# Kernel optimization log

Measured on AMD Instinct MI355X. Metric: run time of the kernel, lower is better.

Reference implementation:

```python
import jax, jax.numpy as jnp
import numpy as np

B, I, J, C = 1, 256, 256, 128
H, D = 4, 32          # no_heads, head_dim; c_hidden = H*D = 128
INF = 1.0e9
LN_EPS = 1e-5


def setup_inputs() -> dict:
    key = jax.random.key(0)
    ks = jax.random.split(key, 8)
    x = jax.random.normal(ks[0], (B, I, J, C), dtype=jnp.float32)
    mask = (jax.random.uniform(ks[1], (B, I, J)) > 0.1).astype(jnp.float32)
    std = 0.02
    wq = std * jax.random.normal(ks[2], (H * D, C), dtype=jnp.float32)
    wk = std * jax.random.normal(ks[3], (H * D, C), dtype=jnp.float32)
    wv = std * jax.random.normal(ks[4], (H * D, C), dtype=jnp.float32)
    wb = std * jax.random.normal(ks[5], (H, C), dtype=jnp.float32)
    wo = (std / np.sqrt(2 * H)) * jax.random.normal(ks[6], (C, H * D), dtype=jnp.float32)
    wo_b = jnp.zeros((C,), dtype=jnp.float32)
    ln_g = jnp.ones((C,), dtype=jnp.float32)
    ln_b = jnp.zeros((C,), dtype=jnp.float32)
    return {"x": x, "mask": mask, "ln_g": ln_g, "ln_b": ln_b,
            "wq": wq, "wk": wk, "wv": wv, "wb": wb, "wo": wo, "wo_b": wo_b}


def reference(x, mask, ln_g, ln_b, wq, wk, wv, wb, wo, wo_b):
    # LayerNorm over channel dim
    mu = jnp.mean(x, axis=-1, keepdims=True)
    var = jnp.mean(jnp.square(x - mu), axis=-1, keepdims=True)
    xn = (x - mu) * jax.lax.rsqrt(var + LN_EPS) * ln_g + ln_b

    # QKV projections (torch Linear: y = x @ W^T), reshape to heads
    q = (xn @ wq.T).reshape(B, I, J, H, D)
    k = (xn @ wk.T).reshape(B, I, J, H, D)
    v = (xn @ wv.T).reshape(B, I, J, H, D)

    scale = 1.0 / np.sqrt(D)
    # attention within each row i over the J dimension: [B, I, H, Jq, Jk]
    scores = jnp.einsum('biqhd,bikhd->bihqk', q, k) * scale

    # triangle bias: [B, I, J, H] -> [B, I, H, Jq, 1], broadcast over keys
    tb = jnp.einsum('bijc,hc->bijh', xn, wb)
    scores = scores + jnp.swapaxes(tb, -1, -2)[..., None]

    # mask bias: inf*(mask-1) -> [B, I, 1, Jq, 1] (as in the torch code)
    scores = scores + (INF * (mask - 1.0))[:, :, None, :, None]

    attn = jax.nn.softmax(scores, axis=-1)
    out = jnp.einsum('bihqk,bikhd->biqhd', attn, v).reshape(B, I, J, H * D)
    return out @ wo.T + wo_b
```

## Files before the change

kernel.cpp:

```cpp
#include <hip/hip_runtime.h>
#include <hip/hip_bf16.h>

typedef short bf16x8 __attribute__((ext_vector_type(8)));
typedef short bf16x4 __attribute__((ext_vector_type(4)));
typedef float f32x4  __attribute__((ext_vector_type(4)));

#define NI 256
#define NJ 256
#define NC 128
#define NH 4
#define ND 32

#define XN_OFF 0
#define XN_STR 272
#define Q_OFF  69632
#define K_OFF  90112
#define QK_STR 80
#define VT_OFF 110592
#define VT_STR 528
#define PB_OFF 127488
#define PB_STR 80
#define TB_OFF 137728
#define MB_OFF 141824
#define SMEM_BYTES 142848

__device__ __forceinline__ short f2bf(float f) {
    return __builtin_bit_cast(short, __float2bfloat16(f));
}
__device__ __forceinline__ float bf2f(short s) {
    unsigned u = ((unsigned)(unsigned short)s) << 16;
    return __builtin_bit_cast(float, u);
}

__global__ __launch_bounds__(512, 2)
void fta_fused(const float* __restrict__ x, const float* __restrict__ mask,
               const float* __restrict__ ln_g, const float* __restrict__ ln_b,
               const float* __restrict__ wq, const float* __restrict__ wk,
               const float* __restrict__ wv, const float* __restrict__ wb,
               const float* __restrict__ wo, const float* __restrict__ wo_b,
               float* __restrict__ out)
{
    extern __shared__ __align__(16) char smem[];
    const int tid  = threadIdx.x;
    const int lane = tid & 63;
    const int wid  = tid >> 6;
    const int g    = lane >> 4;
    const int l16  = lane & 15;
    const int i    = blockIdx.x;

    {
        const int t  = tid >> 1;
        const int ch = (tid & 1) * 64;
        const float* xr = x + ((size_t)i * NJ + t) * NC + ch;
        f32x4 vx[16];
        float s0 = 0.f;
        #pragma unroll
        for (int u = 0; u < 16; ++u) {
            vx[u] = *(const f32x4*)(xr + 4 * u);
            s0 += vx[u][0] + vx[u][1] + vx[u][2] + vx[u][3];
        }
        s0 += __shfl_xor(s0, 1);
        const float mu = s0 * (1.0f / 128.0f);
        float v0 = 0.f;
        #pragma unroll
        for (int u = 0; u < 16; ++u) {
            #pragma unroll
            for (int e = 0; e < 4; ++e) { float d = vx[u][e] - mu; v0 += d * d; }
        }
        v0 += __shfl_xor(v0, 1);
        const float rs = rsqrtf(v0 * (1.0f / 128.0f) + 1e-5f);
        short* xnrow = (short*)(smem + XN_OFF + (size_t)t * XN_STR) + ch;
        #pragma unroll
        for (int u = 0; u < 16; u += 2) {
            f32x4 ga = *(const f32x4*)(ln_g + ch + 4 * u);
            f32x4 gb = *(const f32x4*)(ln_g + ch + 4 * u + 4);
            f32x4 ba = *(const f32x4*)(ln_b + ch + 4 * u);
            f32x4 bb = *(const f32x4*)(ln_b + ch + 4 * u + 4);
            bf16x8 o8;
            #pragma unroll
            for (int e = 0; e < 4; ++e) {
                o8[e]     = f2bf((vx[u][e]     - mu) * rs * ga[e] + ba[e]);
                o8[4 + e] = f2bf((vx[u + 1][e] - mu) * rs * gb[e] + bb[e]);
            }
            *(bf16x8*)(xnrow + 4 * u) = o8;
        }
        if (tid < 256) {
            ((float*)(smem + MB_OFF))[tid] = 1.0e9f * (mask[(size_t)i * NJ + tid] - 1.0f);
        }
    }
    __syncthreads();

    for (int job = tid; job < NH * NJ; job += 512) {
        const int t = job & 255;
        const int h = job >> 8;
        const short* xnrow = (const short*)(smem + XN_OFF + (size_t)t * XN_STR);
        const float* wr = wb + h * NC;
        float acc = 0.f;
        #pragma unroll
        for (int c = 0; c < NC; c += 8) {
            bf16x8 xv = *(const bf16x8*)(xnrow + c);
            f32x4 wa = *(const f32x4*)(wr + c);
            f32x4 wz = *(const f32x4*)(wr + c + 4);
            acc += bf2f(xv[0]) * wa[0] + bf2f(xv[1]) * wa[1] + bf2f(xv[2]) * wa[2] + bf2f(xv[3]) * wa[3]
                 + bf2f(xv[4]) * wz[0] + bf2f(xv[5]) * wz[1] + bf2f(xv[6]) * wz[2] + bf2f(xv[7]) * wz[3];
        }
        ((float*)(smem + TB_OFF))[h * NJ + t] = acc;
    }

    f32x4 facc[2][8];
    #pragma unroll
    for (int qt = 0; qt < 2; ++qt)
        #pragma unroll
        for (int ct = 0; ct < 8; ++ct)
            facc[qt][ct] = (f32x4){0.f, 0.f, 0.f, 0.f};

    const float SCALE = 0.17677669529663687f;
    const f32x4 z4 = {0.f, 0.f, 0.f, 0.f};

    for (int h = 0; h < NH; ++h) {
        __syncthreads();
        for (int chunk = wid; chunk < 12; chunk += 8) {
            const int pn = chunk >> 1;
            const int mhalf = chunk & 1;
            const int p = pn >> 1;
            const int nt2 = pn & 1;
            const float* w = (p == 0) ? wq : ((p == 1) ? wk : wv);
            const int drow = h * ND + nt2 * 16 + l16;
            const float* wrow = w + (size_t)drow * NC + g * 8;
            bf16x8 bfr[4];
            #pragma unroll
            for (int ks = 0; ks < 4; ++ks) {
                f32x4 a = *(const f32x4*)(wrow + ks * 32);
                f32x4 b = *(const f32x4*)(wrow + ks * 32 + 4);
                bf16x8 t8;
                #pragma unroll
                for (int e = 0; e < 4; ++e) { t8[e] = f2bf(a[e]); t8[4 + e] = f2bf(b[e]); }
                bfr[ks] = t8;
            }
            for (int mt = 0; mt < 8; ++mt) {
                const int trow = mhalf * 128 + mt * 16;
                const short* xnr = (const short*)(smem + XN_OFF + (size_t)(trow + l16) * XN_STR) + g * 8;
                f32x4 acc = z4;
                #pragma unroll
                for (int ks = 0; ks < 4; ++ks) {
                    bf16x8 av = *(const bf16x8*)(xnr + ks * 32);
                    acc = __builtin_amdgcn_mfma_f32_16x16x32_bf16(av, bfr[ks], acc, 0, 0, 0);
                }
                const int tt = trow + g * 4;
                const int dd = nt2 * 16 + l16;
                if (p < 2) {
                    char* buf = smem + (p == 0 ? Q_OFF : K_OFF);
                    #pragma unroll
                    for (int r = 0; r < 4; ++r)
                        *((short*)(buf + (size_t)(tt + r) * QK_STR) + dd) = f2bf(acc[r]);
                } else {
                    bf16x4 pk;
                    #pragma unroll
                    for (int r = 0; r < 4; ++r) pk[r] = f2bf(acc[r]);
                    *(bf16x4*)((short*)(smem + VT_OFF + (size_t)dd * VT_STR) + tt) = pk;
                }
            }
        }
        __syncthreads();

        char* pb = smem + PB_OFF + (size_t)wid * 16 * PB_STR;
        #pragma unroll
        for (int qt = 0; qt < 2; ++qt) {
            const int tq = wid * 32 + qt * 16;
            f32x4 tb4 = *(const f32x4*)((const float*)(smem + TB_OFF) + h * NJ + tq + g * 4);
            f32x4 mb4 = *(const f32x4*)((const float*)(smem + MB_OFF) + tq + g * 4);
            f32x4 tbmb;
            #pragma unroll
            for (int e = 0; e < 4; ++e) tbmb[e] = tb4[e] + mb4[e];

            bf16x8 qf = *(const bf16x8*)((const short*)(smem + Q_OFF + (size_t)(tq + l16) * QK_STR) + g * 8);
            f32x4 s[16];
            #pragma unroll
            for (int kt = 0; kt < 16; ++kt) {
                bf16x8 kf = *(const bf16x8*)((const short*)(smem + K_OFF + (size_t)(kt * 16 + l16) * QK_STR) + g * 8);
                s[kt] = __builtin_amdgcn_mfma_f32_16x16x32_bf16(qf, kf, z4, 0, 0, 0);
            }
            #pragma unroll
            for (int kt = 0; kt < 16; ++kt)
                #pragma unroll
                for (int r = 0; r < 4; ++r)
                    s[kt][r] = fmaf(s[kt][r], SCALE, tbmb[r]);

            f32x4 mx = s[0];
            #pragma unroll
            for (int kt = 1; kt < 16; ++kt)
                #pragma unroll
                for (int r = 0; r < 4; ++r) mx[r] = fmaxf(mx[r], s[kt][r]);
            #pragma unroll
            for (int d = 1; d < 16; d <<= 1)
                #pragma unroll
                for (int r = 0; r < 4; ++r) mx[r] = fmaxf(mx[r], __shfl_xor(mx[r], d));

            f32x4 sum = z4;
            #pragma unroll
            for (int kt = 0; kt < 16; ++kt)
                #pragma unroll
                for (int r = 0; r < 4; ++r) { s[kt][r] = __expf(s[kt][r] - mx[r]); sum[r] += s[kt][r]; }
            #pragma unroll
            for (int d = 1; d < 16; d <<= 1)
                #pragma unroll
                for (int r = 0; r < 4; ++r) sum[r] += __shfl_xor(sum[r], d);
            f32x4 inv;
            #pragma unroll
            for (int r = 0; r < 4; ++r) inv[r] = 1.0f / sum[r];
            #pragma unroll
            for (int kt = 0; kt < 16; ++kt)
                #pragma unroll
                for (int r = 0; r < 4; ++r) s[kt][r] *= inv[r];

            f32x4 oacc0 = z4, oacc1 = z4;
            #pragma unroll
            for (int c = 0; c < 8; ++c) {
                #pragma unroll
                for (int kk = 0; kk < 2; ++kk) {
                    const int kt = c * 2 + kk;
                    #pragma unroll
                    for (int r = 0; r < 4; ++r)
                        *((short*)(pb + (size_t)(g * 4 + r) * PB_STR) + kk * 16 + l16) = f2bf(s[kt][r]);
                }
                bf16x8 a   = *(const bf16x8*)((const short*)(pb + (size_t)l16 * PB_STR) + g * 8);
                bf16x8 vb0 = *(const bf16x8*)((const short*)(smem + VT_OFF + (size_t)l16 * VT_STR) + c * 32 + g * 8);
                bf16x8 vb1 = *(const bf16x8*)((const short*)(smem + VT_OFF + (size_t)(16 + l16) * VT_STR) + c * 32 + g * 8);
                oacc0 = __builtin_amdgcn_mfma_f32_16x16x32_bf16(a, vb0, oacc0, 0, 0, 0);
                oacc1 = __builtin_amdgcn_mfma_f32_16x16x32_bf16(a, vb1, oacc1, 0, 0, 0);
            }

            #pragma unroll
            for (int r = 0; r < 4; ++r) {
                *((short*)(pb + (size_t)(g * 4 + r) * PB_STR) + l16)      = f2bf(oacc0[r]);
                *((short*)(pb + (size_t)(g * 4 + r) * PB_STR) + 16 + l16) = f2bf(oacc1[r]);
            }
            bf16x8 oa = *(const bf16x8*)((const short*)(pb + (size_t)l16 * PB_STR) + g * 8);
            #pragma unroll
            for (int ct = 0; ct < 8; ++ct) {
                const float* wrow = wo + (size_t)(ct * 16 + l16) * NC + h * ND + g * 8;
                f32x4 a4 = *(const f32x4*)(wrow);
                f32x4 b4 = *(const f32x4*)(wrow + 4);
                bf16x8 wf;
                #pragma unroll
                for (int e = 0; e < 4; ++e) { wf[e] = f2bf(a4[e]); wf[4 + e] = f2bf(b4[e]); }
                facc[qt][ct] = __builtin_amdgcn_mfma_f32_16x16x32_bf16(oa, wf, facc[qt][ct], 0, 0, 0);
            }
        }
    }

    #pragma unroll
    for (int ct = 0; ct < 8; ++ct) {
        const int col = ct * 16 + l16;
        const float bias = wo_b[col];
        #pragma unroll
        for (int qt = 0; qt < 2; ++qt) {
            const int trow = wid * 32 + qt * 16 + g * 4;
            #pragma unroll
            for (int r = 0; r < 4; ++r)
                out[((size_t)i * NJ + trow + r) * NC + col] = facc[qt][ct][r] + bias;
        }
    }
}

extern "C" void kernel_launch(void* const* d_in, const int* in_sizes, int n_in,
                              void* d_out, int out_size, void* d_ws, size_t ws_size,
                              hipStream_t stream) {
    const float* x    = (const float*)d_in[0];
    const float* mask = (const float*)d_in[1];
    const float* ln_g = (const float*)d_in[2];
    const float* ln_b = (const float*)d_in[3];
    const float* wq   = (const float*)d_in[4];
    const float* wk   = (const float*)d_in[5];
    const float* wv   = (const float*)d_in[6];
    const float* wb   = (const float*)d_in[7];
    const float* wo   = (const float*)d_in[8];
    const float* wo_b = (const float*)d_in[9];
    float* out = (float*)d_out;

    (void)hipFuncSetAttribute((const void*)fta_fused,
                              hipFuncAttributeMaxDynamicSharedMemorySize, SMEM_BYTES);

    fta_fused<<<dim3(NI), dim3(512), SMEM_BYTES, stream>>>(
        x, mask, ln_g, ln_b, wq, wk, wv, wb, wo, wo_b, out);
}
```

Baseline: 86.03 us.

## Split fused kernel into QKV, per-head attention, and output-projection kernels

Replaces the single fused kernel (one 512-thread block per row i, 142KB LDS, serial loop over heads) with three kernels. The first does LayerNorm and the QKV projections per half-row, the second does attention per (row, head), and the third does the output projection. Intermediates go through a global workspace, with async global-to-LDS loads in the later kernels. The goal is more blocks, smaller LDS and higher occupancy. The cost is extra global traffic for Q/K/V and the attention output, plus two more kernel launches.

```diff
diff --git a/kernel.cpp b/kernel.cpp
--- a/kernel.cpp
+++ b/kernel.cpp
@@ -2,8 +2,8 @@
 #include <hip/hip_bf16.h>
 
 typedef short bf16x8 __attribute__((ext_vector_type(8)));
-typedef short bf16x4 __attribute__((ext_vector_type(4)));
 typedef float f32x4  __attribute__((ext_vector_type(4)));
+typedef int   i32x4  __attribute__((ext_vector_type(4)));
 
 #define NI 256
 #define NJ 256
@@ -11,18 +11,15 @@
 #define NH 4
 #define ND 32
 
-#define XN_OFF 0
-#define XN_STR 272
-#define Q_OFF  69632
-#define K_OFF  90112
-#define QK_STR 80
-#define VT_OFF 110592
-#define VT_STR 528
-#define PB_OFF 127488
-#define PB_STR 80
-#define TB_OFF 137728
-#define MB_OFF 141824
-#define SMEM_BYTES 142848
+#define QG_OFF  0
+#define QG_PER  16384
+#define KG_OFF  16777216
+#define KG_PER  20480
+#define VTG_OFF 37748736
+#define VTG_PER 17408
+#define TBM_OFF 55574528
+#define OG_OFF  56623104
+#define WS_NEED 74448896
 
 __device__ __forceinline__ short f2bf(float f) {
     return __builtin_bit_cast(short, __float2bfloat16(f));
@@ -32,68 +29,85 @@
     return __builtin_bit_cast(float, u);
 }
 
-__global__ __launch_bounds__(512, 2)
-void fta_fused(const float* __restrict__ x, const float* __restrict__ mask,
-               const float* __restrict__ ln_g, const float* __restrict__ ln_b,
-               const float* __restrict__ wq, const float* __restrict__ wk,
-               const float* __restrict__ wv, const float* __restrict__ wb,
-               const float* __restrict__ wo, const float* __restrict__ wo_b,
-               float* __restrict__ out)
+typedef __attribute__((address_space(1))) const void gvoid_t;
+typedef __attribute__((address_space(3))) void svoid_t;
+__device__ __forceinline__ void load_lds16(const void* g, void* l) {
+    __builtin_amdgcn_global_load_lds((gvoid_t*)g, (svoid_t*)l, 16, 0, 0);
+}
+
+__global__ __launch_bounds__(512, 4)
+void k_qkv(const float* __restrict__ x, const float* __restrict__ mask,
+           const float* __restrict__ ln_g, const float* __restrict__ ln_b,
+           const float* __restrict__ wq, const float* __restrict__ wk,
+           const float* __restrict__ wv, const float* __restrict__ wb,
+           char* __restrict__ ws)
 {
-    extern __shared__ __align__(16) char smem[];
+    __shared__ short xn[128][136];
+    __shared__ short qs[128][32];
+    __shared__ short ks[128][40];
+    __shared__ short vts[32][132];
+
     const int tid  = threadIdx.x;
     const int lane = tid & 63;
     const int wid  = tid >> 6;
     const int g    = lane >> 4;
     const int l16  = lane & 15;
-    const int i    = blockIdx.x;
+    const int b    = blockIdx.x;
+    const int i    = b >> 1;
+    const int half = b & 1;
+    const int j0   = half * 128;
+
+    short* qg  = (short*)(ws + QG_OFF);
+    short* kg  = (short*)(ws + KG_OFF);
+    short* vtg = (short*)(ws + VTG_OFF);
+    float* tbm = (float*)(ws + TBM_OFF);
 
     {
-        const int t  = tid >> 1;
-        const int ch = (tid & 1) * 64;
-        const float* xr = x + ((size_t)i * NJ + t) * NC + ch;
-        f32x4 vx[16];
+        const int t  = tid >> 2;
+        const int p  = tid & 3;
+        const int ch = p * 32;
+        const float* xr = x + ((size_t)(i * NJ) + j0 + t) * NC + ch;
+        f32x4 vx[8];
         float s0 = 0.f;
         #pragma unroll
-        for (int u = 0; u < 16; ++u) {
+        for (int u = 0; u < 8; ++u) {
             vx[u] = *(const f32x4*)(xr + 4 * u);
             s0 += vx[u][0] + vx[u][1] + vx[u][2] + vx[u][3];
         }
         s0 += __shfl_xor(s0, 1);
+        s0 += __shfl_xor(s0, 2);
         const float mu = s0 * (1.0f / 128.0f);
         float v0 = 0.f;
         #pragma unroll
-        for (int u = 0; u < 16; ++u) {
+        for (int u = 0; u < 8; ++u) {
             #pragma unroll
             for (int e = 0; e < 4; ++e) { float d = vx[u][e] - mu; v0 += d * d; }
         }
         v0 += __shfl_xor(v0, 1);
+        v0 += __shfl_xor(v0, 2);
         const float rs = rsqrtf(v0 * (1.0f / 128.0f) + 1e-5f);
-        short* xnrow = (short*)(smem + XN_OFF + (size_t)t * XN_STR) + ch;
-        #pragma unroll
-        for (int u = 0; u < 16; u += 2) {
-            f32x4 ga = *(const f32x4*)(ln_g + ch + 4 * u);
-            f32x4 gb = *(const f32x4*)(ln_g + ch + 4 * u + 4);
-            f32x4 ba = *(const f32x4*)(ln_b + ch + 4 * u);
-            f32x4 bb = *(const f32x4*)(ln_b + ch + 4 * u + 4);
+        short* xnrow = &xn[t][ch];
+        #pragma unroll
+        for (int u = 0; u < 4; ++u) {
+            f32x4 ga = *(const f32x4*)(ln_g + ch + 8 * u);
+            f32x4 gb = *(const f32x4*)(ln_g + ch + 8 * u + 4);
+            f32x4 ba = *(const f32x4*)(ln_b + ch + 8 * u);
+            f32x4 bb = *(const f32x4*)(ln_b + ch + 8 * u + 4);
             bf16x8 o8;
             #pragma unroll
             for (int e = 0; e < 4; ++e) {
-                o8[e]     = f2bf((vx[u][e]     - mu) * rs * ga[e] + ba[e]);
-                o8[4 + e] = f2bf((vx[u + 1][e] - mu) * rs * gb[e] + bb[e]);
-            }
-            *(bf16x8*)(xnrow + 4 * u) = o8;
-        }
-        if (tid < 256) {
-            ((float*)(smem + MB_OFF))[tid] = 1.0e9f * (mask[(size_t)i * NJ + tid] - 1.0f);
+                o8[e]     = f2bf((vx[2*u][e]   - mu) * rs * ga[e] + ba[e]);
+                o8[4 + e] = f2bf((vx[2*u+1][e] - mu) * rs * gb[e] + bb[e]);
+            }
+            *(bf16x8*)(xnrow + 8 * u) = o8;
         }
     }
     __syncthreads();
 
-    for (int job = tid; job < NH * NJ; job += 512) {
-        const int t = job & 255;
-        const int h = job >> 8;
-        const short* xnrow = (const short*)(smem + XN_OFF + (size_t)t * XN_STR);
+    {
+        const int h = tid >> 7;
+        const int t = tid & 127;
+        const short* xnrow = &xn[t][0];
         const float* wr = wb + h * NC;
         float acc = 0.f;
         #pragma unroll
@@ -104,162 +118,223 @@
             acc += bf2f(xv[0]) * wa[0] + bf2f(xv[1]) * wa[1] + bf2f(xv[2]) * wa[2] + bf2f(xv[3]) * wa[3]
                  + bf2f(xv[4]) * wz[0] + bf2f(xv[5]) * wz[1] + bf2f(xv[6]) * wz[2] + bf2f(xv[7]) * wz[3];
         }
-        ((float*)(smem + TB_OFF))[h * NJ + t] = acc;
-    }
-
-    f32x4 facc[2][8];
-    #pragma unroll
-    for (int qt = 0; qt < 2; ++qt)
-        #pragma unroll
-        for (int ct = 0; ct < 8; ++ct)
-            facc[qt][ct] = (f32x4){0.f, 0.f, 0.f, 0.f};
+        acc += 1.0e9f * (mask[(size_t)i * NJ + j0 + t] - 1.0f);
+        tbm[((size_t)(i * NH) + h) * NJ + j0 + t] = acc;
+    }
+
+    const f32x4 z4 = {0.f, 0.f, 0.f, 0.f};
+
+    for (int h = 0; h < NH; ++h) {
+        #pragma unroll
+        for (int nt = 0; nt < 6; ++nt) {
+            const int p_  = nt >> 1;
+            const int sub = nt & 1;
+            const float* W = (p_ == 0) ? wq : ((p_ == 1) ? wk : wv);
+            const float* wrow = W + (size_t)(h * ND + sub * 16 + l16) * NC + g * 8;
+            bf16x8 bfr[4];
+            #pragma unroll
+            for (int ks_ = 0; ks_ < 4; ++ks_) {
+                f32x4 a = *(const f32x4*)(wrow + ks_ * 32);
+                f32x4 c = *(const f32x4*)(wrow + ks_ * 32 + 4);
+                bf16x8 t8;
+                #pragma unroll
+                for (int e = 0; e < 4; ++e) { t8[e] = f2bf(a[e]); t8[4 + e] = f2bf(c[e]); }
+                bfr[ks_] = t8;
+            }
+            const short* xnr = &xn[wid * 16 + l16][g * 8];
+            f32x4 acc = z4;
+            #pragma unroll
+            for (int ks_ = 0; ks_ < 4; ++ks_) {
+                bf16x8 av = *(const bf16x8*)(xnr + ks_ * 32);
+                acc = __builtin_amdgcn_mfma_f32_16x16x32_bf16(av, bfr[ks_], acc, 0, 0, 0);
+            }
+            const int tok = wid * 16 + g * 4;
+            const int dd  = sub * 16 + l16;
+            if (p_ == 0) {
+                #pragma unroll
+                for (int r = 0; r < 4; ++r) qs[tok + r][dd] = f2bf(acc[r]);
+            } else if (p_ == 1) {
+                #pragma unroll
+                for (int r = 0; r < 4; ++r) ks[tok + r][dd] = f2bf(acc[r]);
+            } else {
+                #pragma unroll
+                for (int r = 0; r < 4; ++r) vts[dd][tok + r] = f2bf(acc[r]);
+            }
+        }
+        __syncthreads();
+
+        const size_t ih = (size_t)(i * NH) + h;
+        for (int job = wid; job < 26; job += 8) {
+            const char* src;
+            char* dst;
+            if (job < 8) {
+                src = (const char*)qs + job * 1024 + lane * 16;
+                dst = (char*)qg + ih * QG_PER + half * 8192 + job * 1024 + lane * 16;
+            } else if (job < 18) {
+                const int jj = job - 8;
+                src = (const char*)ks + jj * 1024 + lane * 16;
+                dst = (char*)kg + ih * KG_PER + half * 10240 + jj * 1024 + lane * 16;
+            } else {
+                const int jj  = job - 18;
+                const int row = jj * 4 + (lane >> 4);
+                const int cb  = (lane & 15) * 16;
+                src = (const char*)vts + row * 264 + cb;
+                dst = (char*)vtg + ih * VTG_PER + row * 528 + half * 256 + cb;
+            }
+            *(i32x4*)dst = *(const i32x4*)src;
+        }
+        __syncthreads();
+    }
+}
+
+__global__ __launch_bounds__(512, 4)
+void k_attn(const char* __restrict__ ws_qkv, short* __restrict__ og)
+{
+    __shared__ short kls[256][40];
+    __shared__ char  vls[17408];
+    __shared__ short pbuf[8][16][40];
+
+    const int tid  = threadIdx.x;
+    const int lane = tid & 63;
+    const int wid  = tid >> 6;
+    const int g    = lane >> 4;
+    const int l16  = lane & 15;
+    const int b    = blockIdx.x;
+    const int i    = b >> 2;
+    const int h    = b & 3;
+    const size_t ih = (size_t)(i * NH) + h;
+
+    const short* qg  = (const short*)(ws_qkv + QG_OFF) + ih * (QG_PER / 2);
+    const char*  kgp = ws_qkv + KG_OFF + ih * KG_PER;
+    const char*  vtp = ws_qkv + VTG_OFF + ih * VTG_PER;
+    const float* tbm = (const float*)(ws_qkv + TBM_OFF) + ih * NJ;
+
+    for (int c = wid; c < 37; c += 8) {
+        if (c < 20) load_lds16(kgp + c * 1024 + lane * 16, (char*)kls + c * 1024);
+        else        load_lds16(vtp + (c - 20) * 1024 + lane * 16, vls + (c - 20) * 1024);
+    }
+    __syncthreads();
 
     const float SCALE = 0.17677669529663687f;
     const f32x4 z4 = {0.f, 0.f, 0.f, 0.f};
-
-    for (int h = 0; h < NH; ++h) {
-        __syncthreads();
-        for (int chunk = wid; chunk < 12; chunk += 8) {
-            const int pn = chunk >> 1;
-            const int mhalf = chunk & 1;
-            const int p = pn >> 1;
-            const int nt2 = pn & 1;
-            const float* w = (p == 0) ? wq : ((p == 1) ? wk : wv);
-            const int drow = h * ND + nt2 * 16 + l16;
-            const float* wrow = w + (size_t)drow * NC + g * 8;
-            bf16x8 bfr[4];
-            #pragma unroll
-            for (int ks = 0; ks < 4; ++ks) {
-                f32x4 a = *(const f32x4*)(wrow + ks * 32);
-                f32x4 b = *(const f32x4*)(wrow + ks * 32 + 4);
-                bf16x8 t8;
-                #pragma unroll
-                for (int e = 0; e < 4; ++e) { t8[e] = f2bf(a[e]); t8[4 + e] = f2bf(b[e]); }
-                bfr[ks] = t8;
-            }
-            for (int mt = 0; mt < 8; ++mt) {
-                const int trow = mhalf * 128 + mt * 16;
-                const short* xnr = (const short*)(smem + XN_OFF + (size_t)(trow + l16) * XN_STR) + g * 8;
-                f32x4 acc = z4;
-                #pragma unroll
-                for (int ks = 0; ks < 4; ++ks) {
-                    bf16x8 av = *(const bf16x8*)(xnr + ks * 32);
-                    acc = __builtin_amdgcn_mfma_f32_16x16x32_bf16(av, bfr[ks], acc, 0, 0, 0);
-                }
-                const int tt = trow + g * 4;
-                const int dd = nt2 * 16 + l16;
-                if (p < 2) {
-                    char* buf = smem + (p == 0 ? Q_OFF : K_OFF);
-                    #pragma unroll
-                    for (int r = 0; r < 4; ++r)
-                        *((short*)(buf + (size_t)(tt + r) * QK_STR) + dd) = f2bf(acc[r]);
-                } else {
-                    bf16x4 pk;
-                    #pragma unroll
-                    for (int r = 0; r < 4; ++r) pk[r] = f2bf(acc[r]);
-                    *(bf16x4*)((short*)(smem + VT_OFF + (size_t)dd * VT_STR) + tt) = pk;
-                }
-            }
-        }
-        __syncthreads();
-
-        char* pb = smem + PB_OFF + (size_t)wid * 16 * PB_STR;
-        #pragma unroll
-        for (int qt = 0; qt < 2; ++qt) {
-            const int tq = wid * 32 + qt * 16;
-            f32x4 tb4 = *(const f32x4*)((const float*)(smem + TB_OFF) + h * NJ + tq + g * 4);
-            f32x4 mb4 = *(const f32x4*)((const float*)(smem + MB_OFF) + tq + g * 4);
-            f32x4 tbmb;
-            #pragma unroll
-            for (int e = 0; e < 4; ++e) tbmb[e] = tb4[e] + mb4[e];
-
-            bf16x8 qf = *(const bf16x8*)((const short*)(smem + Q_OFF + (size_t)(tq + l16) * QK_STR) + g * 8);
-            f32x4 s[16];
-            #pragma unroll
-            for (int kt = 0; kt < 16; ++kt) {
-                bf16x8 kf = *(const bf16x8*)((const short*)(smem + K_OFF + (size_t)(kt * 16 + l16) * QK_STR) + g * 8);
-                s[kt] = __builtin_amdgcn_mfma_f32_16x16x32_bf16(qf, kf, z4, 0, 0, 0);
-            }
-            #pragma unroll
-            for (int kt = 0; kt < 16; ++kt)
+    char* pb = (char*)&pbuf[wid][0][0];
+
+    #pragma unroll
+    for (int qt = 0; qt < 2; ++qt) {
+        const int tq = wid * 32 + qt * 16;
+        f32x4 tbmb = *(const f32x4*)(tbm + tq + g * 4);
+
+        bf16x8 qf = *(const bf16x8*)(qg + (size_t)(tq + l16) * 32 + g * 8);
+        f32x4 s[16];
+        #pragma unroll
+        for (int kt = 0; kt < 16; ++kt) {
+            bf16x8 kf = *(const bf16x8*)(&kls[kt * 16 + l16][g * 8]);
+            s[kt] = __builtin_amdgcn_mfma_f32_16x16x32_bf16(qf, kf, z4, 0, 0, 0);
+        }
+        #pragma unroll
+        for (int kt = 0; kt < 16; ++kt)
+            #pragma unroll
+            for (int r = 0; r < 4; ++r)
+                s[kt][r] = fmaf(s[kt][r], SCALE, tbmb[r]);
+
+        f32x4 mx = s[0];
+        #pragma unroll
+        for (int kt = 1; kt < 16; ++kt)
+            #pragma unroll
+            for (int r = 0; r < 4; ++r) mx[r] = fmaxf(mx[r], s[kt][r]);
+        #pragma unroll
+        for (int d = 1; d < 16; d <<= 1)
+            #pragma unroll
+            for (int r = 0; r < 4; ++r) mx[r] = fmaxf(mx[r], __shfl_xor(mx[r], d));
+
+        f32x4 sum = z4;
+        #pragma unroll
+        for (int kt = 0; kt < 16; ++kt)
+            #pragma unroll
+            for (int r = 0; r < 4; ++r) { s[kt][r] = __expf(s[kt][r] - mx[r]); sum[r] += s[kt][r]; }
+        #pragma unroll
+        for (int d = 1; d < 16; d <<= 1)
+            #pragma unroll
+            for (int r = 0; r < 4; ++r) sum[r] += __shfl_xor(sum[r], d);
+        f32x4 inv;
+        #pragma unroll
+        for (int r = 0; r < 4; ++r) inv[r] = 1.0f / sum[r];
+        #pragma unroll
+        for (int kt = 0; kt < 16; ++kt)
+            #pragma unroll
+            for (int r = 0; r < 4; ++r) s[kt][r] *= inv[r];
+
+        f32x4 oacc0 = z4, oacc1 = z4;
+        #pragma unroll
+        for (int c = 0; c < 8; ++c) {
+            #pragma unroll
+            for (int kk = 0; kk < 2; ++kk) {
+                const int kt = c * 2 + kk;
                 #pragma unroll
                 for (int r = 0; r < 4; ++r)
-                    s[kt][r] = fmaf(s[kt][r], SCALE, tbmb[r]);
-
-            f32x4 mx = s[0];
-            #pragma unroll
-            for (int kt = 1; kt < 16; ++kt)
-                #pragma unroll
-                for (int r = 0; r < 4; ++r) mx[r] = fmaxf(mx[r], s[kt][r]);
-            #pragma unroll
-            for (int d = 1; d < 16; d <<= 1)
-                #pragma unroll
-                for (int r = 0; r < 4; ++r) mx[r] = fmaxf(mx[r], __shfl_xor(mx[r], d));
-
-            f32x4 sum = z4;
-            #pragma unroll
-            for (int kt = 0; kt < 16; ++kt)
-                #pragma unroll
-                for (int r = 0; r < 4; ++r) { s[kt][r] = __expf(s[kt][r] - mx[r]); sum[r] += s[kt][r]; }
-            #pragma unroll
-            for (int d = 1; d < 16; d <<= 1)
-                #pragma unroll
-                for (int r = 0; r < 4; ++r) sum[r] += __shfl_xor(sum[r], d);
-            f32x4 inv;
-            #pragma unroll
-            for (int r = 0; r < 4; ++r) inv[r] = 1.0f / sum[r];
-            #pragma unroll
-            for (int kt = 0; kt < 16; ++kt)
-                #pragma unroll
-                for (int r = 0; r < 4; ++r) s[kt][r] *= inv[r];
-
-            f32x4 oacc0 = z4, oacc1 = z4;
-            #pragma unroll
-            for (int c = 0; c < 8; ++c) {
-                #pragma unroll
-                for (int kk = 0; kk < 2; ++kk) {
-                    const int kt = c * 2 + kk;
-                    #pragma unroll
-                    for (int r = 0; r < 4; ++r)
-                        *((short*)(pb + (size_t)(g * 4 + r) * PB_STR) + kk * 16 + l16) = f2bf(s[kt][r]);
-                }
-                bf16x8 a   = *(const bf16x8*)((const short*)(pb + (size_t)l16 * PB_STR) + g * 8);
-                bf16x8 vb0 = *(const bf16x8*)((const short*)(smem + VT_OFF + (size_t)l16 * VT_STR) + c * 32 + g * 8);
-                bf16x8 vb1 = *(const bf16x8*)((const short*)(smem + VT_OFF + (size_t)(16 + l16) * VT_STR) + c * 32 + g * 8);
-                oacc0 = __builtin_amdgcn_mfma_f32_16x16x32_bf16(a, vb0, oacc0, 0, 0, 0);
-                oacc1 = __builtin_amdgcn_mfma_f32_16x16x32_bf16(a, vb1, oacc1, 0, 0, 0);
-            }
-
-            #pragma unroll
-            for (int r = 0; r < 4; ++r) {
-                *((short*)(pb + (size_t)(g * 4 + r) * PB_STR) + l16)      = f2bf(oacc0[r]);
-                *((short*)(pb + (size_t)(g * 4 + r) * PB_STR) + 16 + l16) = f2bf(oacc1[r]);
-            }
-            bf16x8 oa = *(const bf16x8*)((const short*)(pb + (size_t)l16 * PB_STR) + g * 8);
-            #pragma unroll
-            for (int ct = 0; ct < 8; ++ct) {
-                const float* wrow = wo + (size_t)(ct * 16 + l16) * NC + h * ND + g * 8;
-                f32x4 a4 = *(const f32x4*)(wrow);
-                f32x4 b4 = *(const f32x4*)(wrow + 4);
-                bf16x8 wf;
-                #pragma unroll
-                for (int e = 0; e < 4; ++e) { wf[e] = f2bf(a4[e]); wf[4 + e] = f2bf(b4[e]); }
-                facc[qt][ct] = __builtin_amdgcn_mfma_f32_16x16x32_bf16(oa, wf, facc[qt][ct], 0, 0, 0);
-            }
-        }
-    }
-
+                    *((short*)(pb + (size_t)(g * 4 + r) * 80) + kk * 16 + l16) = f2bf(s[kt][r]);
+            }
+            bf16x8 a   = *(const bf16x8*)((const short*)(pb + (size_t)l16 * 80) + g * 8);
+            bf16x8 vb0 = *(const bf16x8*)((const short*)(vls + (size_t)l16 * 528) + c * 32 + g * 8);
+            bf16x8 vb1 = *(const bf16x8*)((const short*)(vls + (size_t)(16 + l16) * 528) + c * 32 + g * 8);
+            oacc0 = __builtin_amdgcn_mfma_f32_16x16x32_bf16(a, vb0, oacc0, 0, 0, 0);
+            oacc1 = __builtin_amdgcn_mfma_f32_16x16x32_bf16(a, vb1, oacc1, 0, 0, 0);
+        }
+
+        #pragma unroll
+        for (int r = 0; r < 4; ++r) {
+            const size_t row = (size_t)(i * NJ) + tq + g * 4 + r;
+            og[row * 136 + h * 32 + l16]      = f2bf(oacc0[r]);
+            og[row * 136 + h * 32 + 16 + l16] = f2bf(oacc1[r]);
+        }
+    }
+}
+
+__global__ __launch_bounds__(512, 4)
+void k_oproj(const char* __restrict__ ws, const float* __restrict__ wo,
+             const float* __restrict__ wo_b, float* __restrict__ out)
+{
+    __shared__ short ol[128][136];
+
+    const int tid  = threadIdx.x;
+    const int lane = tid & 63;
+    const int wid  = tid >> 6;
+    const int g    = lane >> 4;
+    const int l16  = lane & 15;
+    const size_t tok0 = (size_t)blockIdx.x * 128;
+
+    const char* ogp = ws + OG_OFF + tok0 * 272;
+    for (int c = wid; c < 34; c += 8)
+        load_lds16(ogp + c * 1024 + lane * 16, (char*)ol + c * 1024);
+    __syncthreads();
+
+    const int nt = wid;
+    const float* wrow = wo + (size_t)(nt * 16 + l16) * NC + g * 8;
+    bf16x8 bfr[4];
     #pragma unroll
-    for (int ct = 0; ct < 8; ++ct) {
-        const int col = ct * 16 + l16;
-        const float bias = wo_b[col];
-        #pragma unroll
-        for (int qt = 0; qt < 2; ++qt) {
-            const int trow = wid * 32 + qt * 16 + g * 4;
-            #pragma unroll
-            for (int r = 0; r < 4; ++r)
-                out[((size_t)i * NJ + trow + r) * NC + col] = facc[qt][ct][r] + bias;
-        }
+    for (int ks_ = 0; ks_ < 4; ++ks_) {
+        f32x4 a = *(const f32x4*)(wrow + ks_ * 32);
+        f32x4 c = *(const f32x4*)(wrow + ks_ * 32 + 4);
+        bf16x8 t8;
+        #pragma unroll
+        for (int e = 0; e < 4; ++e) { t8[e] = f2bf(a[e]); t8[4 + e] = f2bf(c[e]); }
+        bfr[ks_] = t8;
+    }
+    const float bias = wo_b[nt * 16 + l16];
+    const f32x4 z4 = {0.f, 0.f, 0.f, 0.f};
+
+    #pragma unroll
+    for (int mt = 0; mt < 8; ++mt) {
+        const short* orow = &ol[mt * 16 + l16][g * 8];
+        f32x4 acc = z4;
+        #pragma unroll
+        for (int ks_ = 0; ks_ < 4; ++ks_) {
+            bf16x8 av = *(const bf16x8*)(orow + ks_ * 32);
+            acc = __builtin_amdgcn_mfma_f32_16x16x32_bf16(av, bfr[ks_], acc, 0, 0, 0);
+        }
+        #pragma unroll
+        for (int r = 0; r < 4; ++r)
+            out[(tok0 + mt * 16 + g * 4 + r) * NC + nt * 16 + l16] = acc[r] + bias;
     }
 }
 
@@ -277,10 +352,9 @@
     const float* wo   = (const float*)d_in[8];
     const float* wo_b = (const float*)d_in[9];
     float* out = (float*)d_out;
-
-    (void)hipFuncSetAttribute((const void*)fta_fused,
-                              hipFuncAttributeMaxDynamicSharedMemorySize, SMEM_BYTES);
-
-    fta_fused<<<dim3(NI), dim3(512), SMEM_BYTES, stream>>>(
-        x, mask, ln_g, ln_b, wq, wk, wv, wb, wo, wo_b, out);
-}
+    char* ws   = (char*)d_ws;
+
+    k_qkv<<<dim3(NI * 2), dim3(512), 0, stream>>>(x, mask, ln_g, ln_b, wq, wk, wv, wb, ws);
+    k_attn<<<dim3(NI * NH), dim3(512), 0, stream>>>(ws, (short*)(ws + OG_OFF));
+    k_oproj<<<dim3(NI * 2), dim3(512), 0, stream>>>(ws, wo, wo_b, out);
+}
```

Measured after the change: 154.0 us. 79.0% more time.
